# Kernel optimization log

Hardware: AMD Instinct MI355X
Metric: run time of the kernel (lower is better)

Reference implementation:

```python
import jax, jax.numpy as jnp
import numpy as np

F = 64          # n_features
H = F * F       # n_hidden = 4096
P = 4           # proj_size
T = 8192        # timesteps


def _proj_lstm_cell_zero_state(x, W_ih, W_hh, b_ih, b_hh, W_hr):
    """One PyTorch proj-LSTM layer applied per-timestep with zero initial
    (h, c). x: [T, in_dim] -> [T, P].  With h0=0, W_hh contributes 0 and
    f*c_prev vanishes."""
    h0 = jnp.zeros((x.shape[0], W_hh.shape[1]), x.dtype)
    gates = x @ W_ih.T + h0 @ W_hh.T + b_ih + b_hh          # [T, 4H]
    i, f, g, o = jnp.split(gates, 4, axis=-1)               # PyTorch gate order
    c = jax.nn.sigmoid(i) * jnp.tanh(g)                     # f*c0 = 0
    h = jax.nn.sigmoid(o) * jnp.tanh(c)                     # [T, H]
    return h @ W_hr.T                                       # [T, P]


def setup_inputs() -> dict:
    key = jax.random.key(0)
    ks = jax.random.split(key, 17)
    s = 0.05
    d = {"x": jax.random.normal(ks[0], (T, F), jnp.float32)}
    shapes = {
        "W_ih_0": (4 * H, F), "W_hh_0": (4 * H, P), "b_ih_0": (4 * H,),
        "b_hh_0": (4 * H,), "W_hr_0": (P, H),
        "W_ih_1": (4 * H, P), "W_hh_1": (4 * H, P), "b_ih_1": (4 * H,),
        "b_hh_1": (4 * H,), "W_hr_1": (P, H),
        "W_ih_2": (4 * H, P), "W_hh_2": (4 * H, P), "b_ih_2": (4 * H,),
        "b_hh_2": (4 * H,), "W_hr_2": (P, H),
    }
    for i, (name, shp) in enumerate(shapes.items()):
        d[name] = s * jax.random.normal(ks[i + 1], shp, jnp.float32)
    return d


def reference(x,
              W_ih_0, W_hh_0, b_ih_0, b_hh_0, W_hr_0,
              W_ih_1, W_hh_1, b_ih_1, b_hh_1, W_hr_1,
              W_ih_2, W_hh_2, b_ih_2, b_hh_2, W_hr_2):
    # study(): inputs.split(1, dim=0) feeds each timestep as a fresh length-1
    # sequence with zero initial state, so timesteps are independent ->
    # vectorize over T instead of the per-step Python loop.
    h = _proj_lstm_cell_zero_state(x, W_ih_0, W_hh_0, b_ih_0, b_hh_0, W_hr_0)
    h = _proj_lstm_cell_zero_state(h, W_ih_1, W_hh_1, b_ih_1, b_hh_1, W_hr_1)
    h = _proj_lstm_cell_zero_state(h, W_ih_2, W_hh_2, b_ih_2, b_hh_2, W_hr_2)
    return h  # [T, P]
```

## Files before the change

kernel.cpp:

```cpp
#include <hip/hip_runtime.h>

#define TSTEPS 8192
#define HDIM 4096
#define PDIM 4
#define KDIM 64

typedef unsigned short u16;
typedef __attribute__((ext_vector_type(8))) short short8;
typedef __attribute__((ext_vector_type(4))) float f32x4;

#define S1 -1.44269504089f
#define S2 -2.88539008177f

#if __has_builtin(__builtin_amdgcn_exp2f)
#define EXP2(x) __builtin_amdgcn_exp2f(x)
#else
#define EXP2(x) exp2f(x)
#endif
__device__ __forceinline__ float rcpf(float x) { return __builtin_amdgcn_rcpf(x); }

__device__ __forceinline__ void gload16(const void* g, void* l) {
  __builtin_amdgcn_global_load_lds((const __attribute__((address_space(1))) unsigned int*)g,
                                   (__attribute__((address_space(3))) unsigned int*)l,
                                   16, 0, 0);
}

__device__ __forceinline__ u16 bf16_rne(float f) {
  unsigned u = __float_as_uint(f);
  u += 0x7FFF + ((u >> 16) & 1);
  return (u16)(u >> 16);
}
__device__ __forceinline__ void hilo(float v, u16& h, u16& l) {
  h = bf16_rne(v);
  l = bf16_rne(v - __uint_as_float((unsigned)h << 16));
}

#define WS_Y0   0
#define WS_Y1   32768
#define WS_BSC  65536
#define WS_C1   77824
#define WS_C2   159744
#define WS_XHI  241664
#define WS_XLO  503808
#define WS_WHI  765952
#define WS_WLO  1159168
#define WS_PP   1552384

__global__ void prep_kernel(const float* __restrict__ x,
                            const float* __restrict__ Wih0, const float* __restrict__ bih0,
                            const float* __restrict__ bhh0,
                            const float* __restrict__ Wih1, const float* __restrict__ bih1,
                            const float* __restrict__ bhh1, const float* __restrict__ Whr1,
                            const float* __restrict__ Wih2, const float* __restrict__ bih2,
                            const float* __restrict__ bhh2, const float* __restrict__ Whr2,
                            float* __restrict__ ws) {
  const int i = blockIdx.x * 256 + threadIdx.x;
  u16* xhi = (u16*)(ws + WS_XHI);
  u16* xlo = (u16*)(ws + WS_XLO);
  u16* whi = (u16*)(ws + WS_WHI);
  u16* wlo = (u16*)(ws + WS_WLO);

  if (i < 131072) {
    float4 v = *(const float4*)&x[i * 4];
    float val[4] = {v.x, v.y, v.z, v.w};
    u16 h[4], l[4];
#pragma unroll
    for (int e = 0; e < 4; ++e) hilo(val[e], h[e], l[e]);
    *(ushort4*)&xhi[i * 4] = make_ushort4(h[0], h[1], h[2], h[3]);
    *(ushort4*)&xlo[i * 4] = make_ushort4(l[0], l[1], l[2], l[3]);
  } else if (i < 327680) {
    int f = i - 131072;
    int el4 = f * 4;
    int r = el4 >> 6;
    int k4 = el4 & 63;
    int gate = r >> 12, jr = r & 4095;
    int src = (gate == 0) ? jr : (gate + 1) * HDIM + jr;
    float sc = (gate == 1) ? S2 : S1;
    float4 v = *(const float4*)&Wih0[(size_t)src * KDIM + k4];
    float val[4] = {sc * v.x, sc * v.y, sc * v.z, sc * v.w};
    u16 h[4], l[4];
#pragma unroll
    for (int e = 0; e < 4; ++e) hilo(val[e], h[e], l[e]);
    *(ushort4*)&whi[r * KDIM + k4] = make_ushort4(h[0], h[1], h[2], h[3]);
    *(ushort4*)&wlo[r * KDIM + k4] = make_ushort4(l[0], l[1], l[2], l[3]);
  } else if (i < 339968) {
    int f = i - 327680;
    int g = f >> 12, j = f & 4095;
    int src = (g == 0) ? j : (g + 1) * HDIM + j;
    float sc = (g == 1) ? S2 : S1;
    ws[WS_BSC + f] = sc * (bih0[src] + bhh0[src]);
  } else if (i < 348160) {
    int f = i - 339968;
    const float* Wih = (f < 4096) ? Wih1 : Wih2;
    const float* bih = (f < 4096) ? bih1 : bih2;
    const float* bhh = (f < 4096) ? bhh1 : bhh2;
    const float* Whr = (f < 4096) ? Whr1 : Whr2;
    float* c = ws + ((f < 4096) ? WS_C1 : WS_C2);
    int j = f & 4095;
    float4 wi = *(const float4*)&Wih[(size_t)j * 4];
    float4 wg = *(const float4*)&Wih[(size_t)(2 * HDIM + j) * 4];
    float4 wo = *(const float4*)&Wih[(size_t)(3 * HDIM + j) * 4];
    float* cb = c + j * 20;
    *(float4*)(cb + 0)  = make_float4(S1 * wi.x, S1 * wi.y, S1 * wi.z, S1 * wi.w);
    *(float4*)(cb + 4)  = make_float4(S2 * wg.x, S2 * wg.y, S2 * wg.z, S2 * wg.w);
    *(float4*)(cb + 8)  = make_float4(S1 * wo.x, S1 * wo.y, S1 * wo.z, S1 * wo.w);
    *(float4*)(cb + 12) = make_float4(S1 * (bih[j] + bhh[j]),
                                      S2 * (bih[2 * HDIM + j] + bhh[2 * HDIM + j]),
                                      S1 * (bih[3 * HDIM + j] + bhh[3 * HDIM + j]), 0.f);
    *(float4*)(cb + 16) = make_float4(Whr[j], Whr[HDIM + j], Whr[2 * HDIM + j], Whr[3 * HDIM + j]);
  }
}

__global__ __launch_bounds__(256, 2)
void lstm_layer0_mfma(const u16* __restrict__ xhi, const u16* __restrict__ xlo,
                      const u16* __restrict__ whi, const u16* __restrict__ wlo,
                      const float* __restrict__ bsc, const float* __restrict__ Whr,
                      float* __restrict__ pp) {
  __shared__ __align__(16) char smem[65536];
  u16* lw_hi = (u16*)smem;
  u16* lw_lo = (u16*)(smem + 24576);
  u16* lx    = (u16*)(smem + 49152);

  const int tid = threadIdx.x;
  const int w = tid >> 6, lane = tid & 63;
  const int m = lane & 15, q = lane >> 4;
  const int jb = blockIdx.x & 63, tbb = blockIdx.x >> 6;
  const int j0 = jb * 64;
  const int t0 = tbb * 256;

  const int r8 = lane >> 3;
  const int swo = ((lane & 7) ^ r8) * 8;

#pragma unroll
  for (int ui = 0; ui < 16; ++ui) {
    const int u = w * 16 + ui;
    const u16* g;
    char* l;
    if (u < 24) {
      g = whi + (size_t)((u >> 3) * HDIM + j0 + (u & 7) * 8 + r8) * 64 + swo;
      l = smem + u * 1024;
    } else if (u < 48) {
      int uu = u - 24;
      g = wlo + (size_t)((uu >> 3) * HDIM + j0 + (uu & 7) * 8 + r8) * 64 + swo;
      l = smem + 24576 + uu * 1024;
    } else {
      int uu = u - 48;
      g = xhi + (size_t)(t0 + uu * 8 + r8) * 64 + swo;
      l = smem + 49152 + uu * 1024;
    }
    gload16(g, l);
  }

  float whr_v[4][4];
#pragma unroll
  for (int p = 0; p < 4; ++p)
#pragma unroll
    for (int js = 0; js < 4; ++js)
      whr_v[p][js] = Whr[(size_t)p * HDIM + j0 + js * 16 + m];
  float biv[4], bgv[4], bov[4];
#pragma unroll
  for (int js = 0; js < 4; ++js) {
    const int j = j0 + js * 16 + m;
    biv[js] = bsc[j];
    bgv[js] = bsc[HDIM + j];
    bov[js] = bsc[2 * HDIM + j];
  }

  f32x4 acc[2][4][3];
  short8 al[2][2];

  auto zero_acc = [&]() {
#pragma unroll
    for (int ts = 0; ts < 2; ++ts)
#pragma unroll
      for (int js = 0; js < 4; ++js)
#pragma unroll
        for (int g = 0; g < 3; ++g) acc[ts][js][g] = (f32x4){0.f, 0.f, 0.f, 0.f};
  };
  auto load_al = [&](int tt) {
#pragma unroll
    for (int kc = 0; kc < 2; ++kc)
#pragma unroll
      for (int ts = 0; ts < 2; ++ts)
        al[kc][ts] = *(const short8*)&xlo[(size_t)(t0 + tt * 128 + w * 32 + ts * 16 + m) * KDIM + kc * 32 + q * 8];
  };
  auto compute = [&]() {
#pragma unroll
    for (int kc = 0; kc < 2; ++kc) {
      const int cs = ((kc * 4 + q) ^ (m & 7)) * 8;
      short8 ah[2];
#pragma unroll
      for (int ts = 0; ts < 2; ++ts)
        ah[ts] = *(const short8*)&lx[(w * 32 + ts * 16 + m) * 64 + cs];
#pragma unroll
      for (int js = 0; js < 4; ++js) {
#pragma unroll
        for (int g = 0; g < 3; ++g) {
          const int roff = (g * 64 + js * 16 + m) * 64 + cs;
          short8 bh = *(const short8*)&lw_hi[roff];
          short8 bl = *(const short8*)&lw_lo[roff];
#pragma unroll
          for (int ts = 0; ts < 2; ++ts) {
            acc[ts][js][g] = __builtin_amdgcn_mfma_f32_16x16x32_bf16(ah[ts], bh, acc[ts][js][g], 0, 0, 0);
            acc[ts][js][g] = __builtin_amdgcn_mfma_f32_16x16x32_bf16(al[kc][ts], bh, acc[ts][js][g], 0, 0, 0);
            acc[ts][js][g] = __builtin_amdgcn_mfma_f32_16x16x32_bf16(ah[ts], bl, acc[ts][js][g], 0, 0, 0);
          }
        }
      }
    }
  };
  auto act_proj = [&](int tt) {
    float hreg[2][4][4];
#pragma unroll
    for (int js = 0; js < 4; ++js) {
#pragma unroll
      for (int ts = 0; ts < 2; ++ts) {
#pragma unroll
        for (int r = 0; r < 4; ++r) {
          float ea = EXP2(acc[ts][js][0][r] + biv[js]);
          float eb = EXP2(acc[ts][js][1][r] + bgv[js]);
          float c = (1.0f - eb) * rcpf((1.0f + ea) * (1.0f + eb));
          float ec = EXP2(acc[ts][js][2][r] + bov[js]);
          float ed = EXP2(S2 * c);
          hreg[ts][js][r] = (1.0f - ed) * rcpf((1.0f + ec) * (1.0f + ed));
        }
      }
    }
#pragma unroll
    for (int ts = 0; ts < 2; ++ts) {
#pragma unroll
      for (int r = 0; r < 4; ++r) {
        float pv[4];
#pragma unroll
        for (int p = 0; p < 4; ++p) {
          float s = 0.f;
#pragma unroll
          for (int js = 0; js < 4; ++js) s = fmaf(hreg[ts][js][r], whr_v[p][js], s);
#pragma unroll
          for (int ofs = 1; ofs < 16; ofs <<= 1) s += __shfl_xor(s, ofs, 16);
          pv[p] = s;
        }
        if (m == 0) {
          const int t = t0 + tt * 128 + w * 32 + ts * 16 + q * 4 + r;
          *(float4*)&pp[((size_t)jb * TSTEPS + t) * PDIM] = make_float4(pv[0], pv[1], pv[2], pv[3]);
        }
      }
    }
  };

  load_al(0);
  zero_acc();
  __syncthreads();
  compute();
  __syncthreads();
#pragma unroll
  for (int ui = 0; ui < 4; ++ui) {
    const int u = w * 4 + ui;
    gload16(xhi + (size_t)(t0 + 128 + u * 8 + r8) * 64 + swo, smem + 49152 + u * 1024);
  }
  load_al(1);
  act_proj(0);
  zero_acc();
  __syncthreads();
  compute();
  act_proj(1);
}

__global__ void reduce64(const float* __restrict__ pp, float* __restrict__ y) {
  const int i = blockIdx.x * 256 + threadIdx.x;
  float s = 0.f;
#pragma unroll 16
  for (int k = 0; k < 64; ++k) s += pp[(size_t)k * (TSTEPS * PDIM) + i];
  y[i] = s;
}

__global__ __launch_bounds__(256, 8)
void lstm_small(const float* __restrict__ xin, const float* __restrict__ cpk,
                float* __restrict__ pp) {
  __shared__ __align__(16) float rec[1280];
  const int tid = threadIdx.x;
  const int tc = blockIdx.x >> 6;
  const int jsp = blockIdx.x & 63;
  const int j0 = jsp * 64;

  for (int i = tid; i < 320; i += 256)
    ((float4*)rec)[i] = ((const float4*)(cpk + (size_t)j0 * 20))[i];

  const int t = tc * 256 + tid;
  float4 xv = ((const float4*)xin)[t];
  float o0 = 0.f, o1 = 0.f, o2 = 0.f, o3 = 0.f;
  __syncthreads();

#pragma unroll 8
  for (int jj = 0; jj < 64; ++jj) {
    const float* cb = rec + jj * 20;
    float4 wi = *(const float4*)(cb + 0);
    float4 wg = *(const float4*)(cb + 4);
    float4 wo = *(const float4*)(cb + 8);
    float4 bb = *(const float4*)(cb + 12);
    float4 wr = *(const float4*)(cb + 16);
    float gi = bb.x, gg = bb.y, go = bb.z;
    gi = fmaf(xv.x, wi.x, gi); gi = fmaf(xv.y, wi.y, gi);
    gi = fmaf(xv.z, wi.z, gi); gi = fmaf(xv.w, wi.w, gi);
    gg = fmaf(xv.x, wg.x, gg); gg = fmaf(xv.y, wg.y, gg);
    gg = fmaf(xv.z, wg.z, gg); gg = fmaf(xv.w, wg.w, gg);
    go = fmaf(xv.x, wo.x, go); go = fmaf(xv.y, wo.y, go);
    go = fmaf(xv.z, wo.z, go); go = fmaf(xv.w, wo.w, go);
    float ea = EXP2(gi), eb = EXP2(gg);
    float c = (1.0f - eb) * rcpf((1.0f + ea) * (1.0f + eb));
    float ec = EXP2(go), ed = EXP2(S2 * c);
    float h = (1.0f - ed) * rcpf((1.0f + ec) * (1.0f + ed));
    o0 = fmaf(h, wr.x, o0); o1 = fmaf(h, wr.y, o1);
    o2 = fmaf(h, wr.z, o2); o3 = fmaf(h, wr.w, o3);
  }

  ((float4*)pp)[(size_t)jsp * TSTEPS + t] = make_float4(o0, o1, o2, o3);
}

extern "C" void kernel_launch(void* const* d_in, const int* in_sizes, int n_in,
                              void* d_out, int out_size, void* d_ws, size_t ws_size,
                              hipStream_t stream) {
  const float* x    = (const float*)d_in[0];
  const float* Wih0 = (const float*)d_in[1];
  const float* bih0 = (const float*)d_in[3];
  const float* bhh0 = (const float*)d_in[4];
  const float* Whr0 = (const float*)d_in[5];
  const float* Wih1 = (const float*)d_in[6];
  const float* bih1 = (const float*)d_in[8];
  const float* bhh1 = (const float*)d_in[9];
  const float* Whr1 = (const float*)d_in[10];
  const float* Wih2 = (const float*)d_in[11];
  const float* bih2 = (const float*)d_in[13];
  const float* bhh2 = (const float*)d_in[14];
  const float* Whr2 = (const float*)d_in[15];
  float* out = (float*)d_out;
  float* ws = (float*)d_ws;
  float* pp = ws + WS_PP;

  prep_kernel<<<dim3(1360), dim3(256), 0, stream>>>(
      x, Wih0, bih0, bhh0, Wih1, bih1, bhh1, Whr1, Wih2, bih2, bhh2, Whr2, ws);

  lstm_layer0_mfma<<<dim3(2048), dim3(256), 0, stream>>>(
      (const u16*)(ws + WS_XHI), (const u16*)(ws + WS_XLO),
      (const u16*)(ws + WS_WHI), (const u16*)(ws + WS_WLO),
      ws + WS_BSC, Whr0, pp);
  reduce64<<<dim3(128), dim3(256), 0, stream>>>(pp, ws + WS_Y0);

  lstm_small<<<dim3(2048), dim3(256), 0, stream>>>(ws + WS_Y0, ws + WS_C1, pp);
  reduce64<<<dim3(128), dim3(256), 0, stream>>>(pp, ws + WS_Y1);

  lstm_small<<<dim3(2048), dim3(256), 0, stream>>>(ws + WS_Y1, ws + WS_C2, pp);
  reduce64<<<dim3(128), dim3(256), 0, stream>>>(pp, out);
}
```

Baseline: 232.8 us.

## Replace tanh(c) with Pade approximant and process two timesteps per thread

Swaps the exp-based tanh of the cell state for a rational Pade approximant merged with the output-gate sigmoid, which saves one exp2 and folds the two denominators into one reciprocal, in both the layer-0 MFMA kernel and the small-layer kernel. The small-layer kernel now handles two timesteps per thread, reusing each LDS weight load across both, and software-prefetches the next hidden unit's weights. Its grid is halved to match. The Pade form is an approximation that loses accuracy when |c| is large, though c stays within (-1,1) here. The prefetch reads one record past the end of the 1280 floats that are loaded (rec is enlarged to 1300, so the read is in bounds but those values are unused).

```diff
diff --git a/kernel.cpp b/kernel.cpp
--- a/kernel.cpp
+++ b/kernel.cpp
@@ -18,6 +18,13 @@
 #define EXP2(x) exp2f(x)
 #endif
 __device__ __forceinline__ float rcpf(float x) { return __builtin_amdgcn_rcpf(x); }
+
+__device__ __forceinline__ float h_merge(float c, float ec) {
+  float c2 = c * c;
+  float num = c * fmaf(c2, 10.0f, 105.0f);
+  float den = fmaf(c2, 45.0f, 105.0f) + c2 * c2;
+  return num * rcpf(den * (1.0f + ec));
+}
 
 __device__ __forceinline__ void gload16(const void* g, void* l) {
   __builtin_amdgcn_global_load_lds((const __attribute__((address_space(1))) unsigned int*)g,
@@ -128,8 +135,8 @@
   const int j0 = jb * 64;
   const int t0 = tbb * 256;
 
-  const int r8 = lane >> 3;
-  const int swo = ((lane & 7) ^ r8) * 8;
+  const int r8_ = lane >> 3;
+  const int swo = ((lane & 7) ^ r8_) * 8;
 
 #pragma unroll
   for (int ui = 0; ui < 16; ++ui) {
@@ -137,15 +144,15 @@
     const u16* g;
     char* l;
     if (u < 24) {
-      g = whi + (size_t)((u >> 3) * HDIM + j0 + (u & 7) * 8 + r8) * 64 + swo;
+      g = whi + (size_t)((u >> 3) * HDIM + j0 + (u & 7) * 8 + r8_) * 64 + swo;
       l = smem + u * 1024;
     } else if (u < 48) {
       int uu = u - 24;
-      g = wlo + (size_t)((uu >> 3) * HDIM + j0 + (uu & 7) * 8 + r8) * 64 + swo;
+      g = wlo + (size_t)((uu >> 3) * HDIM + j0 + (uu & 7) * 8 + r8_) * 64 + swo;
       l = smem + 24576 + uu * 1024;
     } else {
       int uu = u - 48;
-      g = xhi + (size_t)(t0 + uu * 8 + r8) * 64 + swo;
+      g = xhi + (size_t)(t0 + uu * 8 + r8_) * 64 + swo;
       l = smem + 49152 + uu * 1024;
     }
     gload16(g, l);
@@ -221,8 +228,7 @@
           float eb = EXP2(acc[ts][js][1][r] + bgv[js]);
           float c = (1.0f - eb) * rcpf((1.0f + ea) * (1.0f + eb));
           float ec = EXP2(acc[ts][js][2][r] + bov[js]);
-          float ed = EXP2(S2 * c);
-          hreg[ts][js][r] = (1.0f - ed) * rcpf((1.0f + ec) * (1.0f + ed));
+          hreg[ts][js][r] = h_merge(c, ec);
         }
       }
     }
@@ -256,7 +262,7 @@
 #pragma unroll
   for (int ui = 0; ui < 4; ++ui) {
     const int u = w * 4 + ui;
-    gload16(xhi + (size_t)(t0 + 128 + u * 8 + r8) * 64 + swo, smem + 49152 + u * 1024);
+    gload16(xhi + (size_t)(t0 + 128 + u * 8 + r8_) * 64 + swo, smem + 49152 + u * 1024);
   }
   load_al(1);
   act_proj(0);
@@ -274,10 +280,9 @@
   y[i] = s;
 }
 
-__global__ __launch_bounds__(256, 8)
-void lstm_small(const float* __restrict__ xin, const float* __restrict__ cpk,
-                float* __restrict__ pp) {
-  __shared__ __align__(16) float rec[1280];
+__global__ void lstm_small(const float* __restrict__ xin, const float* __restrict__ cpk,
+                           float* __restrict__ pp) {
+  __shared__ __align__(16) float rec[1300];
   const int tid = threadIdx.x;
   const int tc = blockIdx.x >> 6;
   const int jsp = blockIdx.x & 63;
@@ -286,35 +291,57 @@
   for (int i = tid; i < 320; i += 256)
     ((float4*)rec)[i] = ((const float4*)(cpk + (size_t)j0 * 20))[i];
 
-  const int t = tc * 256 + tid;
-  float4 xv = ((const float4*)xin)[t];
-  float o0 = 0.f, o1 = 0.f, o2 = 0.f, o3 = 0.f;
+  const int ta = tc * 512 + tid;
+  const int tb2 = ta + 256;
+  float4 xa = ((const float4*)xin)[ta];
+  float4 xb = ((const float4*)xin)[tb2];
+  float a0 = 0.f, a1 = 0.f, a2 = 0.f, a3 = 0.f;
+  float b0 = 0.f, b1 = 0.f, b2 = 0.f, b3 = 0.f;
   __syncthreads();
 
-#pragma unroll 8
+  float4 wi = *(const float4*)(rec + 0);
+  float4 wg = *(const float4*)(rec + 4);
+  float4 wo = *(const float4*)(rec + 8);
+  float4 bb = *(const float4*)(rec + 12);
+  float4 wr = *(const float4*)(rec + 16);
+
+#pragma unroll 2
   for (int jj = 0; jj < 64; ++jj) {
-    const float* cb = rec + jj * 20;
-    float4 wi = *(const float4*)(cb + 0);
-    float4 wg = *(const float4*)(cb + 4);
-    float4 wo = *(const float4*)(cb + 8);
-    float4 bb = *(const float4*)(cb + 12);
-    float4 wr = *(const float4*)(cb + 16);
+    const float* nb = rec + (jj + 1) * 20;
+    float4 nwi = *(const float4*)(nb + 0);
+    float4 nwg = *(const float4*)(nb + 4);
+    float4 nwo = *(const float4*)(nb + 8);
+    float4 nbb = *(const float4*)(nb + 12);
+    float4 nwr = *(const float4*)(nb + 16);
     float gi = bb.x, gg = bb.y, go = bb.z;
-    gi = fmaf(xv.x, wi.x, gi); gi = fmaf(xv.y, wi.y, gi);
-    gi = fmaf(xv.z, wi.z, gi); gi = fmaf(xv.w, wi.w, gi);
-    gg = fmaf(xv.x, wg.x, gg); gg = fmaf(xv.y, wg.y, gg);
-    gg = fmaf(xv.z, wg.z, gg); gg = fmaf(xv.w, wg.w, gg);
-    go = fmaf(xv.x, wo.x, go); go = fmaf(xv.y, wo.y, go);
-    go = fmaf(xv.z, wo.z, go); go = fmaf(xv.w, wo.w, go);
+    gi = fmaf(xa.x, wi.x, gi); gi = fmaf(xa.y, wi.y, gi);
+    gi = fmaf(xa.z, wi.z, gi); gi = fmaf(xa.w, wi.w, gi);
+    gg = fmaf(xa.x, wg.x, gg); gg = fmaf(xa.y, wg.y, gg);
+    gg = fmaf(xa.z, wg.z, gg); gg = fmaf(xa.w, wg.w, gg);
+    go = fmaf(xa.x, wo.x, go); go = fmaf(xa.y, wo.y, go);
+    go = fmaf(xa.z, wo.z, go); go = fmaf(xa.w, wo.w, go);
     float ea = EXP2(gi), eb = EXP2(gg);
     float c = (1.0f - eb) * rcpf((1.0f + ea) * (1.0f + eb));
-    float ec = EXP2(go), ed = EXP2(S2 * c);
-    float h = (1.0f - ed) * rcpf((1.0f + ec) * (1.0f + ed));
-    o0 = fmaf(h, wr.x, o0); o1 = fmaf(h, wr.y, o1);
-    o2 = fmaf(h, wr.z, o2); o3 = fmaf(h, wr.w, o3);
-  }
-
-  ((float4*)pp)[(size_t)jsp * TSTEPS + t] = make_float4(o0, o1, o2, o3);
+    float h = h_merge(c, EXP2(go));
+    a0 = fmaf(h, wr.x, a0); a1 = fmaf(h, wr.y, a1);
+    a2 = fmaf(h, wr.z, a2); a3 = fmaf(h, wr.w, a3);
+    gi = bb.x; gg = bb.y; go = bb.z;
+    gi = fmaf(xb.x, wi.x, gi); gi = fmaf(xb.y, wi.y, gi);
+    gi = fmaf(xb.z, wi.z, gi); gi = fmaf(xb.w, wi.w, gi);
+    gg = fmaf(xb.x, wg.x, gg); gg = fmaf(xb.y, wg.y, gg);
+    gg = fmaf(xb.z, wg.z, gg); gg = fmaf(xb.w, wg.w, gg);
+    go = fmaf(xb.x, wo.x, go); go = fmaf(xb.y, wo.y, go);
+    go = fmaf(xb.z, wo.z, go); go = fmaf(xb.w, wo.w, go);
+    ea = EXP2(gi); eb = EXP2(gg);
+    c = (1.0f - eb) * rcpf((1.0f + ea) * (1.0f + eb));
+    h = h_merge(c, EXP2(go));
+    b0 = fmaf(h, wr.x, b0); b1 = fmaf(h, wr.y, b1);
+    b2 = fmaf(h, wr.z, b2); b3 = fmaf(h, wr.w, b3);
+    wi = nwi; wg = nwg; wo = nwo; bb = nbb; wr = nwr;
+  }
+
+  ((float4*)pp)[(size_t)jsp * TSTEPS + ta]  = make_float4(a0, a1, a2, a3);
+  ((float4*)pp)[(size_t)jsp * TSTEPS + tb2] = make_float4(b0, b1, b2, b3);
 }
 
 extern "C" void kernel_launch(void* const* d_in, const int* in_sizes, int n_in,
@@ -346,9 +373,9 @@
       ws + WS_BSC, Whr0, pp);
   reduce64<<<dim3(128), dim3(256), 0, stream>>>(pp, ws + WS_Y0);
 
-  lstm_small<<<dim3(2048), dim3(256), 0, stream>>>(ws + WS_Y0, ws + WS_C1, pp);
+  lstm_small<<<dim3(1024), dim3(256), 0, stream>>>(ws + WS_Y0, ws + WS_C1, pp);
   reduce64<<<dim3(128), dim3(256), 0, stream>>>(pp, ws + WS_Y1);
 
-  lstm_small<<<dim3(2048), dim3(256), 0, stream>>>(ws + WS_Y1, ws + WS_C2, pp);
+  lstm_small<<<dim3(1024), dim3(256), 0, stream>>>(ws + WS_Y1, ws + WS_C2, pp);
   reduce64<<<dim3(128), dim3(256), 0, stream>>>(pp, out);
 }
```

Result: slower. 237.4 us (+2.0%).
